# Kernel optimization log

Hardware: AMD Instinct MI355X
Metric: run time of the kernel (lower is better)

## Reference

```python
import jax, jax.numpy as jnp
import numpy as np

N_NODES = 50000


def graph_conv(h, src, dst, W, b, num_nodes):
    """GCN-style conv: transform node features, then sum messages over edges.
    h: [N, Din], W: [Din, Dout] -> out: [N, Dout].
    """
    m = (h @ W)[src]                                   # [E, Dout] per-edge messages
    agg = jax.ops.segment_sum(m, dst, num_segments=num_nodes)  # [N, Dout]
    return agg + b


def setup_inputs() -> dict:
    key = jax.random.key(0)
    ks = jax.random.split(key, 8)
    N, E, D = N_NODES, 800000, 128
    s = 1.0 / np.sqrt(2 * D)
    return {
        "node_feature": jax.random.normal(ks[0], (N, D), jnp.float32),
        "H_prev": jax.random.normal(ks[1], (N, D), jnp.float32),
        "edge_index": jax.random.randint(ks[2], (2, E), 0, N, jnp.int32),
        "W_main": jax.random.normal(ks[3], (D, D), jnp.float32) / np.sqrt(D),
        "b_main": jnp.zeros((D,), jnp.float32),
        "W_z": jax.random.normal(ks[4], (2 * D, D), jnp.float32) * s,
        "b_z": jnp.zeros((D,), jnp.float32),
        "W_r": jax.random.normal(ks[5], (2 * D, D), jnp.float32) * s,
        "b_r": jnp.zeros((D,), jnp.float32),
        "W_h": jax.random.normal(ks[6], (2 * D, D), jnp.float32) * s,
        "b_h": jnp.zeros((D,), jnp.float32),
    }


def reference(node_feature, H_prev, edge_index, W_main, b_main,
              W_z, b_z, W_r, b_r, W_h, b_h):
    N = node_feature.shape[0]
    src, dst = edge_index[0], edge_index[1]
    # main message-passing layer + post-layer activation (ReLU)
    X = jax.nn.relu(graph_conv(node_feature, src, dst, W_main, b_main, N))
    # GRU-gated graph convolutions
    cat_zr = jnp.concatenate([X, H_prev], axis=1)       # [N, 2D]
    Z = jax.nn.sigmoid(graph_conv(cat_zr, src, dst, W_z, b_z, N))
    R = jax.nn.sigmoid(graph_conv(cat_zr, src, dst, W_r, b_r, N))
    cat_h = jnp.concatenate([X, R * H_prev], axis=1)
    H_tilde = jnp.tanh(graph_conv(cat_h, src, dst, W_h, b_h, N))
    H_out = Z * H_prev + (1.0 - Z) * H_tilde
    return H_out
```

## Files before the change

kernel.cpp:

```cpp
#include <hip/hip_runtime.h>
#include <hip/hip_fp16.h>
#include <math.h>

typedef _Float16 f16;
typedef f16 f16x2 __attribute__((ext_vector_type(2)));
typedef f16 f16x4 __attribute__((ext_vector_type(4)));
typedef f16 f16x8 __attribute__((ext_vector_type(8)));
typedef float f32x4_t __attribute__((ext_vector_type(4)));

__device__ __forceinline__ float sigmoidf(float x) {
  return 1.0f / (1.0f + __expf(-x));
}

#define GLDS16(gp, lp)                                                     \
  __builtin_amdgcn_global_load_lds(                                        \
      (const __attribute__((address_space(1))) void*)(gp),                 \
      (__attribute__((address_space(3))) void*)(lp), 16, 0, 0)

__global__ void zero_ints(int* __restrict__ p, int n) {
  int i = blockIdx.x * blockDim.x + threadIdx.x;
  if (i < n) p[i] = 0;
}

__global__ __launch_bounds__(256) void bucket_hist2(const int* __restrict__ dst,
                                                    int* __restrict__ hrows, int E) {
  __shared__ int h[256];
  h[threadIdx.x] = 0;
  __syncthreads();
  int base = blockIdx.x * 4096;
  int lim = min(base + 4096, E);
  for (int e = base + threadIdx.x; e < lim; e += 256)
    atomicAdd(&h[dst[e] >> 8], 1);
  __syncthreads();
  hrows[blockIdx.x * 256 + threadIdx.x] = h[threadIdx.x];
}

__global__ __launch_bounds__(256) void bucket_scan2(const int* __restrict__ hrows,
                                                    int nhb, int* __restrict__ bbases,
                                                    int* __restrict__ gcurP, int NB) {
  __shared__ int wsum[4];
  const int tid = threadIdx.x, lane = tid & 63, wid = tid >> 6;
  int v = 0;
  for (int b = 0; b < nhb; ++b) v += hrows[b * 256 + tid];
  if (tid >= NB) v = 0;
  int x = v;
  #pragma unroll
  for (int d = 1; d < 64; d <<= 1) { int y = __shfl_up(x, d); if (lane >= d) x += y; }
  if (lane == 63) wsum[wid] = x;
  __syncthreads();
  if (wid == 0 && lane < 4) {
    int ws = wsum[lane];
    #pragma unroll
    for (int d = 1; d < 4; d <<= 1) { int y = __shfl_up(ws, d); if (lane >= d) ws += y; }
    wsum[lane] = ws;
  }
  __syncthreads();
  int excl = x - v + (wid ? wsum[wid - 1] : 0);
  if (tid < NB) { bbases[tid] = excl; gcurP[tid * 16] = excl; }
  if (tid == NB - 1) bbases[NB] = excl + v;
}

__global__ __launch_bounds__(256) void partition_v2(const int* __restrict__ src,
                                                    const int* __restrict__ dst,
                                                    int* __restrict__ gcurP,
                                                    unsigned int* __restrict__ bin,
                                                    int E, int NB) {
  __shared__ int bhist[256];
  __shared__ int bofs[257];
  __shared__ int gbase[256];
  __shared__ unsigned int recs[4096];
  const int tid = threadIdx.x;
  const int base = blockIdx.x * 4096;
  bhist[tid] = 0;
  __syncthreads();
  unsigned int rec[16];
  int bk[16];
  #pragma unroll
  for (int k = 0; k < 16; ++k) {
    int e = base + tid + k * 256;
    if (e < E) {
      int d = dst[e];
      rec[k] = (unsigned int)(src[e] & 0xFFFF) | ((unsigned int)(d & 255) << 16);
      bk[k] = d >> 8;
      atomicAdd(&bhist[bk[k]], 1);
    } else {
      bk[k] = -1;
    }
  }
  __syncthreads();
  if (tid < 64) {
    int l = tid;
    int v0 = bhist[4 * l], v1 = bhist[4 * l + 1];
    int v2 = bhist[4 * l + 2], v3 = bhist[4 * l + 3];
    int s1 = v0 + v1, s2 = s1 + v2, t = s2 + v3;
    int x = t;
    #pragma unroll
    for (int d = 1; d < 64; d <<= 1) { int y = __shfl_up(x, d); if (l >= d) x += y; }
    int basex = x - t;
    bofs[4 * l] = basex;
    bofs[4 * l + 1] = basex + v0;
    bofs[4 * l + 2] = basex + s1;
    bofs[4 * l + 3] = basex + s2;
    if (l == 63) bofs[256] = x;
  }
  __syncthreads();
  if (tid < NB && bhist[tid] > 0)
    gbase[tid] = atomicAdd(&gcurP[tid * 16], bhist[tid]);
  bhist[tid] = bofs[tid];
  __syncthreads();
  #pragma unroll
  for (int k = 0; k < 16; ++k) {
    if (bk[k] >= 0) {
      int p = atomicAdd(&bhist[bk[k]], 1);
      recs[p] = rec[k];
    }
  }
  __syncthreads();
  const int total = bofs[256];
  for (int i = tid; i < total; i += 256) {
    int lo = 0, hi = 256;
    #pragma unroll
    for (int s = 0; s < 8; ++s) {
      int mid = (lo + hi) >> 1;
      if (bofs[mid] <= i) lo = mid; else hi = mid;
    }
    bin[gbase[lo] + (i - bofs[lo])] = recs[i];
  }
}

__global__ __launch_bounds__(256) void bucket_sort(const unsigned int* __restrict__ bin,
                                                   const int* __restrict__ bbases,
                                                   unsigned short* __restrict__ eidx,
                                                   int* __restrict__ off,
                                                   int N, int NB) {
  const int b = blockIdx.x;
  const int bb = bbases[b], be = bbases[b + 1];
  const int cntb = be - bb;
  const int d0 = b << 8;
  const int ndst = min(256, N - d0);
  __shared__ int hist[256];
  __shared__ int lofs[256];
  __shared__ int cnt2[256];
  __shared__ unsigned short srt[8192];
  const int tid = threadIdx.x;
  hist[tid] = 0;
  cnt2[tid] = 0;
  __syncthreads();
  for (int i = bb + tid; i < be; i += 256)
    atomicAdd(&hist[(bin[i] >> 16) & 255], 1);
  __syncthreads();
  if (tid < 64) {
    int l = tid;
    int v0 = hist[4 * l], v1 = hist[4 * l + 1], v2 = hist[4 * l + 2], v3 = hist[4 * l + 3];
    int s1 = v0 + v1, s2 = s1 + v2, t = s2 + v3;
    int x = t;
    #pragma unroll
    for (int d = 1; d < 64; d <<= 1) { int y = __shfl_up(x, d); if (l >= d) x += y; }
    int basex = x - t;
    lofs[4 * l] = basex;
    lofs[4 * l + 1] = basex + v0;
    lofs[4 * l + 2] = basex + s1;
    lofs[4 * l + 3] = basex + s2;
  }
  __syncthreads();
  if (tid < ndst) off[d0 + tid] = bb + lofs[tid];
  if (b == NB - 1 && tid == 0) off[N] = be;
  if (cntb <= 8192) {
    for (int i = bb + tid; i < be; i += 256) {
      unsigned int r = bin[i];
      int ld = (r >> 16) & 255;
      int p = lofs[ld] + atomicAdd(&cnt2[ld], 1);
      srt[p] = (unsigned short)(r & 0xFFFF);
    }
    __syncthreads();
    for (int i = tid; i < cntb; i += 256) eidx[bb + i] = srt[i];
  } else {
    for (int i = bb + tid; i < be; i += 256) {
      unsigned int r = bin[i];
      int ld = (r >> 16) & 255;
      int p = bb + lofs[ld] + atomicAdd(&cnt2[ld], 1);
      eidx[p] = (unsigned short)(r & 0xFFFF);
    }
  }
}

__global__ void count_kernel(const int* __restrict__ dst, int* __restrict__ cnt, int E) {
  int base = (blockIdx.x * blockDim.x + threadIdx.x) * 4;
  if (base + 3 < E) {
    int4 d = *(const int4*)&dst[base];
    atomicAdd(&cnt[d.x], 1);
    atomicAdd(&cnt[d.y], 1);
    atomicAdd(&cnt[d.z], 1);
    atomicAdd(&cnt[d.w], 1);
  } else {
    for (int e = base; e < E; ++e) atomicAdd(&cnt[dst[e]], 1);
  }
}

__global__ __launch_bounds__(1024) void scan_local(const int* __restrict__ cnt,
                                                   int* __restrict__ off,
                                                   int* __restrict__ psum, int n) {
  __shared__ int wsum[16];
  const int tid = threadIdx.x, lane = tid & 63, wid = tid >> 6;
  int i = blockIdx.x * 1024 + tid;
  int v = (i < n) ? cnt[i] : 0;
  int x = v;
  #pragma unroll
  for (int d = 1; d < 64; d <<= 1) { int y = __shfl_up(x, d); if (lane >= d) x += y; }
  if (lane == 63) wsum[wid] = x;
  __syncthreads();
  if (wid == 0) {
    int ws = (lane < 16) ? wsum[lane] : 0;
    #pragma unroll
    for (int d = 1; d < 16; d <<= 1) { int y = __shfl_up(ws, d); if (lane >= d) ws += y; }
    if (lane < 16) wsum[lane] = ws;
  }
  __syncthreads();
  int excl = x - v + (wid ? wsum[wid - 1] : 0);
  if (i < n) off[i] = excl;
  if (tid == 1023) psum[blockIdx.x] = wsum[15];
}

__global__ __launch_bounds__(1024) void scan_carry(int* __restrict__ psum,
                                                   int* __restrict__ off,
                                                   int* __restrict__ cur, int nb, int n) {
  __shared__ int wsum[16];
  const int tid = threadIdx.x, lane = tid & 63, wid = tid >> 6;
  int v = (tid < nb) ? psum[tid] : 0;
  int x = v;
  #pragma unroll
  for (int d = 1; d < 64; d <<= 1) { int y = __shfl_up(x, d); if (lane >= d) x += y; }
  if (lane == 63) wsum[wid] = x;
  __syncthreads();
  if (wid == 0) {
    int ws = (lane < 16) ? wsum[lane] : 0;
    #pragma unroll
    for (int d = 1; d < 16; d <<= 1) { int y = __shfl_up(ws, d); if (lane >= d) ws += y; }
    if (lane < 16) wsum[lane] = ws;
  }
  __syncthreads();
  int excl = x - v + (wid ? wsum[wid - 1] : 0);
  if (tid < nb) psum[tid] = excl;
  if (tid == 1023) { off[n] = wsum[15]; cur[n] = wsum[15]; }
}

__global__ __launch_bounds__(1024) void scan_add(int* __restrict__ off, int* __restrict__ cur,
                                                 const int* __restrict__ psum, int n) {
  int i = blockIdx.x * 1024 + threadIdx.x;
  if (i < n) {
    int t = off[i] + psum[blockIdx.x];
    off[i] = t;
    cur[i] = t;
  }
}

__global__ void fill_kernel(const int* __restrict__ src, const int* __restrict__ dst,
                            int* __restrict__ cur, int* __restrict__ eidx, int E) {
  int base = (blockIdx.x * blockDim.x + threadIdx.x) * 4;
  if (base + 3 < E) {
    int4 d = *(const int4*)&dst[base];
    int4 s = *(const int4*)&src[base];
    int p0 = atomicAdd(&cur[d.x], 1);
    int p1 = atomicAdd(&cur[d.y], 1);
    int p2 = atomicAdd(&cur[d.z], 1);
    int p3 = atomicAdd(&cur[d.w], 1);
    eidx[p0] = s.x; eidx[p1] = s.y; eidx[p2] = s.z; eidx[p3] = s.w;
  } else {
    for (int e = base; e < E; ++e) {
      int p = atomicAdd(&cur[dst[e]], 1);
      eidx[p] = src[e];
    }
  }
}

__global__ __launch_bounds__(256) void prep_kernel(
    const float* __restrict__ Wm, const float* __restrict__ Wz,
    const float* __restrict__ Wr, const float* __restrict__ Wh,
    f16* __restrict__ WtM, f16* __restrict__ WtZR, f16* __restrict__ WtH,
    const float* __restrict__ nf, const float* __restrict__ H,
    f16* __restrict__ P0, int N) {
  const int bid = blockIdx.x;
  if (bid < 128) {
    __shared__ float tile[32][33];
    const int t = bid;
    const int x = t & 7, y = (t >> 3) & 3, z = t >> 5;
    const float* W;
    f16* O;
    int K;
    switch (z) {
      case 0: W = Wm; O = WtM; K = 128; break;
      case 1: W = Wz; O = WtZR; K = 256; break;
      case 2: W = Wr; O = WtZR + 128 * 256; K = 256; break;
      default: W = Wh; O = WtH; K = 256; break;
    }
    int bk = x * 32, bn = y * 32;
    if (bk >= K) return;
    int tx = threadIdx.x & 31, ty = threadIdx.x >> 5;
    #pragma unroll
    for (int i = 0; i < 4; ++i)
      tile[ty + 8 * i][tx] = W[(size_t)(bk + ty + 8 * i) * 128 + bn + tx];
    __syncthreads();
    #pragma unroll
    for (int i = 0; i < 4; ++i)
      O[(size_t)(bn + ty + 8 * i) * K + bk + tx] = (f16)tile[tx][ty + 8 * i];
  } else {
    const int w = (bid - 128) * 4 + (threadIdx.x >> 6);
    if (w >= N) return;
    int lane = threadIdx.x & 63;
    const float* S = (lane < 32) ? nf : H;
    int c = (lane & 31) * 4;
    float4 u = *(const float4*)&S[(size_t)w * 128 + c];
    f16x4 o = {(f16)u.x, (f16)u.y, (f16)u.z, (f16)u.w};
    *(f16x4*)&P0[(size_t)w * 256 + (lane < 32 ? 0 : 128) + c] = o;
  }
}

template <int COLS, typename IDX>
__global__ __launch_bounds__(256) void gather(const f16* __restrict__ P,
                                              const int* __restrict__ off,
                                              const IDX* __restrict__ eidx,
                                              f16* __restrict__ O, int N) {
  constexpr int NG = (COLS == 256) ? 2 : 4;
  constexpr int GL = 64 / NG;
  constexpr int SH = (COLS == 256) ? 9 : 8;
  int gid = blockIdx.x * blockDim.x + threadIdx.x;
  int wave = gid >> 6;
  int lane = threadIdx.x & 63;
  int g = lane / GL, lg = lane % GL;
  int node = wave * NG + g;
  if (node >= N) return;
  const int beg = off[node], end = off[node + 1];
  const char* base = (const char*)P + lg * 16;
  float a0 = 0.f, a1 = 0.f, a2 = 0.f, a3 = 0.f;
  float a4 = 0.f, a5 = 0.f, a6 = 0.f, a7 = 0.f;
  int j = beg;
  for (; j + 8 <= end; j += 8) {
    f16x8 v[8];
    #pragma unroll
    for (int u = 0; u < 8; ++u)
      v[u] = *(const f16x8*)(base + (((int)eidx[j + u]) << SH));
    #pragma unroll
    for (int u = 0; u < 8; ++u) {
      a0 += (float)v[u][0]; a1 += (float)v[u][1];
      a2 += (float)v[u][2]; a3 += (float)v[u][3];
      a4 += (float)v[u][4]; a5 += (float)v[u][5];
      a6 += (float)v[u][6]; a7 += (float)v[u][7];
    }
  }
  for (; j < end; ++j) {
    f16x8 v = *(const f16x8*)(base + (((int)eidx[j]) << SH));
    a0 += (float)v[0]; a1 += (float)v[1]; a2 += (float)v[2]; a3 += (float)v[3];
    a4 += (float)v[4]; a5 += (float)v[5]; a6 += (float)v[6]; a7 += (float)v[7];
  }
  f16x8 o = {(f16)a0, (f16)a1, (f16)a2, (f16)a3, (f16)a4, (f16)a5, (f16)a6, (f16)a7};
  *(f16x8*)&O[(size_t)node * COLS + lg * 8] = o;
}

template <int TERMS, int EPI>
__global__ __launch_bounds__(256) void gemm_mfma(
    const f16* __restrict__ A0, int lda0, const f16* __restrict__ A1, int lda1,
    const f16* __restrict__ Wt,
    const float* __restrict__ b0, const float* __restrict__ b1,
    const float* __restrict__ H, const f16* __restrict__ Zh,
    f16* __restrict__ O0, f16* __restrict__ O1, float* __restrict__ Ofp, int N) {
  constexpr int KTOT = TERMS * 128;
  constexpr int T = KTOT / 64;
  __shared__ __align__(16) f16 As[2][64][64];
  __shared__ __align__(16) f16 Bs[2][128][64];
  const int tid = threadIdx.x;
  const int l = tid & 63;
  const int wv = __builtin_amdgcn_readfirstlane(tid >> 6);
  const int fr = l & 15;
  const int q = l >> 4;
  const int brow = blockIdx.x * 64;
  const int coff = blockIdx.y * 128;
  const int rowA = wv * 16 + fr;
  const int sl8 = l >> 3, sg = l & 7;

  f32x4_t acc[8];
  #pragma unroll
  for (int n = 0; n < 8; ++n) acc[n] = (f32x4_t)0.0f;

  auto stage = [&](int t, int buf) {
    const bool sel1 = (TERMS == 2) && (t >= 2);
    const f16* __restrict__ A = sel1 ? A1 : A0;
    const int lda = sel1 ? lda1 : lda0;
    const int klocal = (t & 1) * 64;
    const int kk = t * 64;
    f16* Asf = &As[buf][0][0];
    f16* Bsf = &Bs[buf][0][0];
    #pragma unroll
    for (int c = 0; c < 2; ++c) {
      int chunk = wv + c * 4;
      int row = chunk * 8 + sl8;
      int gs = sg ^ (row & 7);
      int grow = brow + row;
      if (grow > N - 1) grow = N - 1;
      GLDS16(A + (size_t)grow * lda + klocal + gs * 8, Asf + chunk * 512);
    }
    #pragma unroll
    for (int c = 0; c < 4; ++c) {
      int chunk = wv + c * 4;
      int col = chunk * 8 + sl8;
      int gs = sg ^ (col & 7);
      GLDS16(Wt + (size_t)(coff + col) * KTOT + kk + gs * 8, Bsf + chunk * 512);
    }
  };

  stage(0, 0);
  #pragma unroll
  for (int t = 0; t < T; ++t) {
    if (t + 1 < T) {
      stage(t + 1, (t + 1) & 1);
      asm volatile("s_waitcnt vmcnt(6)" ::: "memory");
    } else {
      asm volatile("s_waitcnt vmcnt(0)" ::: "memory");
    }
    __builtin_amdgcn_s_barrier();
    const int buf = t & 1;
    #pragma unroll
    for (int ks = 0; ks < 2; ++ks) {
      f16x8 a = *(const f16x8*)&As[buf][rowA][((ks * 4 + q) ^ (rowA & 7)) * 8];
      f16x8 bfr[8];
      #pragma unroll
      for (int n = 0; n < 8; ++n) {
        int colB = n * 16 + fr;
        bfr[n] = *(const f16x8*)&Bs[buf][colB][((ks * 4 + q) ^ (colB & 7)) * 8];
      }
      #pragma unroll
      for (int n = 0; n < 8; ++n)
        acc[n] = __builtin_amdgcn_mfma_f32_16x16x32_f16(a, bfr[n], acc[n], 0, 0, 0);
    }
    asm volatile("s_waitcnt lgkmcnt(0)" ::: "memory");
    __builtin_amdgcn_s_barrier();
  }

  const int row0 = brow + wv * 16 + q * 4;
  #pragma unroll
  for (int n = 0; n < 8; ++n) {
    int colL = n * 16 + fr;
    if (EPI == 0) {
      float bias = b0[colL];
      #pragma unroll
      for (int r = 0; r < 4; ++r) {
        int row = row0 + r;
        if (row < N)
          O0[(size_t)row * 128 + colL] = (f16)fmaxf(acc[n][r] + bias, 0.f);
      }
    } else if (EPI == 1) {
      if (coff == 0) {
        float bias = b0[colL];
        #pragma unroll
        for (int r = 0; r < 4; ++r) {
          int row = row0 + r;
          if (row < N)
            O0[(size_t)row * 128 + colL] = (f16)sigmoidf(acc[n][r] + bias);
        }
      } else {
        float bias = b1[colL];
        #pragma unroll
        for (int r = 0; r < 4; ++r) {
          int row = row0 + r;
          if (row < N) {
            float g = sigmoidf(acc[n][r] + bias) * H[(size_t)row * 128 + colL];
            O1[(size_t)row * 128 + colL] = (f16)g;
          }
        }
      }
    } else {
      float bias = b0[colL];
      #pragma unroll
      for (int r = 0; r < 4; ++r) {
        int row = row0 + r;
        if (row < N) {
          size_t p = (size_t)row * 128 + colL;
          float ht = tanhf(acc[n][r] + bias);
          float z = (float)Zh[p];
          float h = H[p];
          Ofp[p] = z * h + (1.0f - z) * ht;
        }
      }
    }
  }
}


extern "C" void kernel_launch(void* const* d_in, const int* in_sizes, int n_in,
                              void* d_out, int out_size, void* d_ws, size_t ws_size,
                              hipStream_t stream) {
  const float* nf = (const float*)d_in[0];
  const float* H  = (const float*)d_in[1];
  const int*   ei = (const int*)d_in[2];
  const float* Wm = (const float*)d_in[3];
  const float* bm = (const float*)d_in[4];
  const float* Wz = (const float*)d_in[5];
  const float* bz = (const float*)d_in[6];
  const float* Wr = (const float*)d_in[7];
  const float* br = (const float*)d_in[8];
  const float* Wh = (const float*)d_in[9];
  const float* bh = (const float*)d_in[10];
  float* out = (float*)d_out;

  const int N = in_sizes[0] / 128;
  const int E = in_sizes[2] / 2;
  const int* src = ei;
  const int* dst = ei + E;

  char* ws = (char*)d_ws;
  size_t o = 0;
  auto alloc = [&](size_t bytes) {
    char* p = ws + o;
    o = (o + bytes + 511) & ~(size_t)511;
    return p;
  };
  const int NB = (N + 255) >> 8;
  const int nhb = (E + 4095) / 4096;
  const int nbch = (N + 1023) / 1024;
  int* hrows  = (int*)alloc((size_t)nhb * 256 * 4);
  int* gcurP  = (int*)alloc((size_t)NB * 16 * 4);
  int* bbases = (int*)alloc((size_t)(NB + 1) * 4);
  unsigned int* bin = (unsigned int*)alloc((size_t)E * 4);
  int* off    = (int*)alloc((size_t)(N + 1) * 4);
  int* cur    = (int*)alloc((size_t)(N + 1) * 4);
  int* cnt    = (int*)alloc((size_t)N * 4);
  int* psum   = (int*)alloc((size_t)nbch * 4);
  void* eidx  = (void*)alloc((size_t)E * 4);
  f16* WtM    = (f16*)alloc((size_t)128 * 128 * 2);
  f16* WtZR   = (f16*)alloc((size_t)256 * 256 * 2);
  f16* WtH    = (f16*)alloc((size_t)128 * 256 * 2);
  f16* P0     = (f16*)alloc((size_t)N * 256 * 2);
  f16* X      = (f16*)alloc((size_t)N * 128 * 2);
  f16* AX     = (f16*)alloc((size_t)N * 128 * 2);
  f16* G      = (f16*)alloc((size_t)N * 128 * 2);
  f16* AP0    = (f16*)d_out;
  f16* Zh     = X;
  f16* AG     = P0;

  const bool small = (N <= 65536);

  if (small) {
    bucket_hist2<<<nhb, 256, 0, stream>>>(dst, hrows, E);
    bucket_scan2<<<1, 256, 0, stream>>>(hrows, nhb, bbases, gcurP, NB);
    partition_v2<<<nhb, 256, 0, stream>>>(src, dst, gcurP, bin, E, NB);
    bucket_sort<<<NB, 256, 0, stream>>>(bin, bbases, (unsigned short*)eidx, off, N, NB);
  } else {
    const int qblk = ((E + 3) / 4 + 255) / 256;
    zero_ints<<<(N + 255) / 256, 256, 0, stream>>>(cnt, N);
    count_kernel<<<qblk, 256, 0, stream>>>(dst, cnt, E);
    scan_local<<<nbch, 1024, 0, stream>>>(cnt, off, psum, N);
    scan_carry<<<1, 1024, 0, stream>>>(psum, off, cur, nbch, N);
    scan_add<<<nbch, 1024, 0, stream>>>(off, cur, psum, N);
    fill_kernel<<<qblk, 256, 0, stream>>>(src, dst, cur, (int*)eidx, E);
  }

  prep_kernel<<<128 + (N + 3) / 4, 256, 0, stream>>>(
      Wm, Wz, Wr, Wh, WtM, WtZR, WtH, nf, H, P0, N);

  const int mblk = (N + 63) / 64;
  const int g256 = (N + 7) / 8;
  const int g128 = (N + 15) / 16;

  if (small)
    gather<256, unsigned short><<<g256, 256, 0, stream>>>(P0, off, (const unsigned short*)eidx, AP0, N);
  else
    gather<256, int><<<g256, 256, 0, stream>>>(P0, off, (const int*)eidx, AP0, N);

  gemm_mfma<1, 0><<<dim3(mblk, 1), 256, 0, stream>>>(
      AP0, 256, nullptr, 0, WtM, bm, nullptr, nullptr, nullptr, X, nullptr, nullptr, N);

  if (small)
    gather<128, unsigned short><<<g128, 256, 0, stream>>>(X, off, (const unsigned short*)eidx, AX, N);
  else
    gather<128, int><<<g128, 256, 0, stream>>>(X, off, (const int*)eidx, AX, N);

  gemm_mfma<2, 1><<<dim3(mblk, 2), 256, 0, stream>>>(
      AX, 128, AP0 + 128, 256, WtZR, bz, br, H, nullptr, Zh, G, nullptr, N);

  if (small)
    gather<128, unsigned short><<<g128, 256, 0, stream>>>(G, off, (const unsigned short*)eidx, AG, N);
  else
    gather<128, int><<<g128, 256, 0, stream>>>(G, off, (const int*)eidx, AG, N);

  gemm_mfma<2, 2><<<dim3(mblk, 1), 256, 0, stream>>>(
      AX, 128, AG, 128, WtH, bh, nullptr, H, Zh, nullptr, nullptr, out, N);
}
```

Baseline: 288.9 us.

## Fuse CSR build and weight/feature prep into one cooperative kernel

Result: slower. 367.1 us (+27.1%).

```diff
diff --git a/kernel.cpp b/kernel.cpp
--- a/kernel.cpp
+++ b/kernel.cpp
@@ -1,4 +1,5 @@
 #include <hip/hip_runtime.h>
+#include <hip/hip_cooperative_groups.h>
 #include <hip/hip_fp16.h>
 #include <math.h>
 
@@ -20,6 +21,204 @@
 __global__ void zero_ints(int* __restrict__ p, int n) {
   int i = blockIdx.x * blockDim.x + threadIdx.x;
   if (i < n) p[i] = 0;
+}
+
+__global__ __launch_bounds__(256) void csr_prep_coop(
+    const int* __restrict__ src, const int* __restrict__ dst, int E, int N,
+    int NB, int nhb, int* __restrict__ hrows, int* __restrict__ bbases,
+    int* __restrict__ gcurP, unsigned int* __restrict__ bin,
+    unsigned short* __restrict__ eidx, int* __restrict__ off,
+    const float* __restrict__ Wm, const float* __restrict__ Wz,
+    const float* __restrict__ Wr, const float* __restrict__ Wh,
+    f16* __restrict__ WtM, f16* __restrict__ WtZR, f16* __restrict__ WtH,
+    const float* __restrict__ nf, const float* __restrict__ H,
+    f16* __restrict__ P0) {
+  cooperative_groups::grid_group grid = cooperative_groups::this_grid();
+  const int b = blockIdx.x, tid = threadIdx.x;
+  __shared__ int h[256];
+  __shared__ int bofs[257];
+  __shared__ int gbase[256];
+  __shared__ int wsum4[4];
+  __shared__ unsigned int recs[4096];
+  __shared__ unsigned short srt[8192];
+  __shared__ int lofs[256];
+  __shared__ int cnt2s[256];
+  __shared__ float tile[32][33];
+
+  unsigned int rec[16];
+  int bk[16];
+  h[tid] = 0;
+  __syncthreads();
+  if (b < nhb) {
+    const int base = b * 4096;
+    #pragma unroll
+    for (int k = 0; k < 16; ++k) {
+      int e = base + tid + k * 256;
+      if (e < E) {
+        int d = dst[e];
+        rec[k] = (unsigned int)(src[e] & 0xFFFF) | ((unsigned int)(d & 255) << 16);
+        bk[k] = d >> 8;
+        atomicAdd(&h[bk[k]], 1);
+      } else {
+        bk[k] = -1;
+      }
+    }
+  } else {
+    #pragma unroll
+    for (int k = 0; k < 16; ++k) bk[k] = -1;
+  }
+  __syncthreads();
+  if (b < nhb) hrows[(size_t)b * 256 + tid] = h[tid];
+
+  if (b < 128) {
+    const int x = b & 7, y = (b >> 3) & 3, z = b >> 5;
+    const float* W;
+    f16* O;
+    int K;
+    switch (z) {
+      case 0: W = Wm; O = WtM; K = 128; break;
+      case 1: W = Wz; O = WtZR; K = 256; break;
+      case 2: W = Wr; O = WtZR + 128 * 256; K = 256; break;
+      default: W = Wh; O = WtH; K = 256; break;
+    }
+    int bkk = x * 32, bn = y * 32;
+    if (bkk < K) {
+      int tx = tid & 31, ty = tid >> 5;
+      #pragma unroll
+      for (int i = 0; i < 4; ++i)
+        tile[ty + 8 * i][tx] = W[(size_t)(bkk + ty + 8 * i) * 128 + bn + tx];
+      __syncthreads();
+      #pragma unroll
+      for (int i = 0; i < 4; ++i)
+        O[(size_t)(bn + ty + 8 * i) * K + bkk + tx] = (f16)tile[tx][ty + 8 * i];
+    }
+  }
+  {
+    const int wv = tid >> 6, lane = tid & 63;
+    const float* S = (lane < 32) ? nf : H;
+    const int c = (lane & 31) * 4;
+    const int coloff = (lane < 32) ? 0 : 128;
+    for (int w = b * 4 + wv; w < N; w += gridDim.x * 4) {
+      float4 u = *(const float4*)&S[(size_t)w * 128 + c];
+      f16x4 o = {(f16)u.x, (f16)u.y, (f16)u.z, (f16)u.w};
+      *(f16x4*)&P0[(size_t)w * 256 + coloff + c] = o;
+    }
+  }
+
+  grid.sync();
+
+  if (b == 0) {
+    int v = 0;
+    for (int b2 = 0; b2 < nhb; ++b2) v += hrows[(size_t)b2 * 256 + tid];
+    if (tid >= NB) v = 0;
+    const int lane = tid & 63, wid = tid >> 6;
+    int x = v;
+    #pragma unroll
+    for (int d = 1; d < 64; d <<= 1) { int y = __shfl_up(x, d); if (lane >= d) x += y; }
+    if (lane == 63) wsum4[wid] = x;
+    __syncthreads();
+    if (wid == 0 && lane < 4) {
+      int wsv = wsum4[lane];
+      #pragma unroll
+      for (int d = 1; d < 4; d <<= 1) { int y = __shfl_up(wsv, d); if (lane >= d) wsv += y; }
+      wsum4[lane] = wsv;
+    }
+    __syncthreads();
+    int excl = x - v + (wid ? wsum4[wid - 1] : 0);
+    if (tid < NB) { bbases[tid] = excl; gcurP[tid * 16] = excl; }
+    if (tid == NB - 1) bbases[NB] = excl + v;
+  }
+
+  grid.sync();
+
+  if (b < nhb) {
+    if (tid < 64) {
+      int l = tid;
+      int v0 = h[4 * l], v1 = h[4 * l + 1], v2 = h[4 * l + 2], v3 = h[4 * l + 3];
+      int s1 = v0 + v1, s2 = s1 + v2, t = s2 + v3;
+      int x = t;
+      #pragma unroll
+      for (int d = 1; d < 64; d <<= 1) { int y = __shfl_up(x, d); if (l >= d) x += y; }
+      int basex = x - t;
+      bofs[4 * l] = basex;
+      bofs[4 * l + 1] = basex + v0;
+      bofs[4 * l + 2] = basex + s1;
+      bofs[4 * l + 3] = basex + s2;
+      if (l == 63) bofs[256] = x;
+    }
+    __syncthreads();
+    if (tid < NB && h[tid] > 0)
+      gbase[tid] = atomicAdd(&gcurP[tid * 16], h[tid]);
+    __syncthreads();
+    h[tid] = bofs[tid];
+    __syncthreads();
+    #pragma unroll
+    for (int k = 0; k < 16; ++k) {
+      if (bk[k] >= 0) {
+        int p = atomicAdd(&h[bk[k]], 1);
+        recs[p] = rec[k];
+      }
+    }
+    __syncthreads();
+    const int total = bofs[256];
+    for (int i = tid; i < total; i += 256) {
+      int lo = 0, hi = 256;
+      #pragma unroll
+      for (int s = 0; s < 8; ++s) {
+        int mid = (lo + hi) >> 1;
+        if (bofs[mid] <= i) lo = mid; else hi = mid;
+      }
+      bin[gbase[lo] + (i - bofs[lo])] = recs[i];
+    }
+  }
+
+  grid.sync();
+
+  if (b < NB) {
+    const int bb = bbases[b], be = bbases[b + 1];
+    const int cntb = be - bb;
+    const int d0 = b << 8;
+    const int ndst = min(256, N - d0);
+    h[tid] = 0;
+    cnt2s[tid] = 0;
+    __syncthreads();
+    for (int i = bb + tid; i < be; i += 256)
+      atomicAdd(&h[(bin[i] >> 16) & 255], 1);
+    __syncthreads();
+    if (tid < 64) {
+      int l = tid;
+      int v0 = h[4 * l], v1 = h[4 * l + 1], v2 = h[4 * l + 2], v3 = h[4 * l + 3];
+      int s1 = v0 + v1, s2 = s1 + v2, t = s2 + v3;
+      int x = t;
+      #pragma unroll
+      for (int d = 1; d < 64; d <<= 1) { int y = __shfl_up(x, d); if (l >= d) x += y; }
+      int basex = x - t;
+      lofs[4 * l] = basex;
+      lofs[4 * l + 1] = basex + v0;
+      lofs[4 * l + 2] = basex + s1;
+      lofs[4 * l + 3] = basex + s2;
+    }
+    __syncthreads();
+    if (tid < ndst) off[d0 + tid] = bb + lofs[tid];
+    if (b == NB - 1 && tid == 0) off[N] = be;
+    if (cntb <= 8192) {
+      for (int i = bb + tid; i < be; i += 256) {
+        unsigned int r = bin[i];
+        int ld = (r >> 16) & 255;
+        int p = lofs[ld] + atomicAdd(&cnt2s[ld], 1);
+        srt[p] = (unsigned short)(r & 0xFFFF);
+      }
+      __syncthreads();
+      for (int i = tid; i < cntb; i += 256) eidx[bb + i] = srt[i];
+    } else {
+      for (int i = bb + tid; i < be; i += 256) {
+        unsigned int r = bin[i];
+        int ld = (r >> 16) & 255;
+        int p = bb + lofs[ld] + atomicAdd(&cnt2s[ld], 1);
+        eidx[p] = (unsigned short)(r & 0xFFFF);
+      }
+    }
+  }
 }
 
 __global__ __launch_bounds__(256) void bucket_hist2(const int* __restrict__ dst,
@@ -106,6 +305,7 @@
   __syncthreads();
   if (tid < NB && bhist[tid] > 0)
     gbase[tid] = atomicAdd(&gcurP[tid * 16], bhist[tid]);
+  __syncthreads();
   bhist[tid] = bofs[tid];
   __syncthreads();
   #pragma unroll
@@ -361,7 +561,7 @@
     const f16* __restrict__ A0, int lda0, const f16* __restrict__ A1, int lda1,
     const f16* __restrict__ Wt,
     const float* __restrict__ b0, const float* __restrict__ b1,
-    const float* __restrict__ H, const f16* __restrict__ Zh,
+    const f16* __restrict__ Hh, const f16* __restrict__ Zh,
     f16* __restrict__ O0, f16* __restrict__ O1, float* __restrict__ Ofp, int N) {
   constexpr int KTOT = TERMS * 128;
   constexpr int T = KTOT / 64;
@@ -462,7 +662,8 @@
         for (int r = 0; r < 4; ++r) {
           int row = row0 + r;
           if (row < N) {
-            float g = sigmoidf(acc[n][r] + bias) * H[(size_t)row * 128 + colL];
+            float hv = (float)Hh[(size_t)row * 256 + colL];
+            float g = sigmoidf(acc[n][r] + bias) * hv;
             O1[(size_t)row * 128 + colL] = (f16)g;
           }
         }
@@ -473,11 +674,10 @@
       for (int r = 0; r < 4; ++r) {
         int row = row0 + r;
         if (row < N) {
-          size_t p = (size_t)row * 128 + colL;
           float ht = tanhf(acc[n][r] + bias);
-          float z = (float)Zh[p];
-          float h = H[p];
-          Ofp[p] = z * h + (1.0f - z) * ht;
+          float z = (float)Zh[(size_t)row * 128 + colL];
+          float hv = (float)Hh[(size_t)row * 256 + colL];
+          Ofp[(size_t)row * 128 + colL] = z * hv + (1.0f - z) * ht;
         }
       }
     }
@@ -532,29 +732,59 @@
   f16* X      = (f16*)alloc((size_t)N * 128 * 2);
   f16* AX     = (f16*)alloc((size_t)N * 128 * 2);
   f16* G      = (f16*)alloc((size_t)N * 128 * 2);
+  f16* AG     = (f16*)alloc((size_t)N * 128 * 2);
   f16* AP0    = (f16*)d_out;
   f16* Zh     = X;
-  f16* AG     = P0;
+  const f16* Hh = P0 + 128;
 
   const bool small = (N <= 65536);
 
+  bool coop_done = false;
   if (small) {
-    bucket_hist2<<<nhb, 256, 0, stream>>>(dst, hrows, E);
-    bucket_scan2<<<1, 256, 0, stream>>>(hrows, nhb, bbases, gcurP, NB);
-    partition_v2<<<nhb, 256, 0, stream>>>(src, dst, gcurP, bin, E, NB);
-    bucket_sort<<<NB, 256, 0, stream>>>(bin, bbases, (unsigned short*)eidx, off, N, NB);
-  } else {
-    const int qblk = ((E + 3) / 4 + 255) / 256;
-    zero_ints<<<(N + 255) / 256, 256, 0, stream>>>(cnt, N);
-    count_kernel<<<qblk, 256, 0, stream>>>(dst, cnt, E);
-    scan_local<<<nbch, 1024, 0, stream>>>(cnt, off, psum, N);
-    scan_carry<<<1, 1024, 0, stream>>>(psum, off, cur, nbch, N);
-    scan_add<<<nbch, 1024, 0, stream>>>(off, cur, psum, N);
-    fill_kernel<<<qblk, 256, 0, stream>>>(src, dst, cur, (int*)eidx, E);
-  }
-
-  prep_kernel<<<128 + (N + 3) / 4, 256, 0, stream>>>(
-      Wm, Wz, Wr, Wh, WtM, WtZR, WtH, nf, H, P0, N);
+    const int NBLK = (nhb > NB) ? nhb : NB;
+    const int* src_a = src; const int* dst_a = dst;
+    int E_a = E, N_a = N, NB_a = NB, nhb_a = nhb;
+    unsigned short* eidx_a = (unsigned short*)eidx;
+    const float* Wm_a = Wm; const float* Wz_a = Wz;
+    const float* Wr_a = Wr; const float* Wh_a = Wh;
+    const float* nf_a = nf; const float* H_a = H;
+    f16* WtM_a = WtM; f16* WtZR_a = WtZR; f16* WtH_a = WtH; f16* P0_a = P0;
+    int* hrows_a = hrows; int* bbases_a = bbases; int* gcurP_a = gcurP;
+    unsigned int* bin_a = bin; int* off_a = off;
+    void* kargs[] = {
+      (void*)&src_a, (void*)&dst_a, (void*)&E_a, (void*)&N_a,
+      (void*)&NB_a, (void*)&nhb_a, (void*)&hrows_a, (void*)&bbases_a,
+      (void*)&gcurP_a, (void*)&bin_a, (void*)&eidx_a, (void*)&off_a,
+      (void*)&Wm_a, (void*)&Wz_a, (void*)&Wr_a, (void*)&Wh_a,
+      (void*)&WtM_a, (void*)&WtZR_a, (void*)&WtH_a,
+      (void*)&nf_a, (void*)&H_a, (void*)&P0_a
+    };
+    hipError_t ce = hipLaunchCooperativeKernel((const void*)csr_prep_coop,
+                                               dim3(NBLK), dim3(256), kargs, 0, stream);
+    if (ce == hipSuccess) {
+      coop_done = true;
+    } else {
+      (void)hipGetLastError();
+    }
+  }
+  if (!coop_done) {
+    if (small) {
+      bucket_hist2<<<nhb, 256, 0, stream>>>(dst, hrows, E);
+      bucket_scan2<<<1, 256, 0, stream>>>(hrows, nhb, bbases, gcurP, NB);
+      partition_v2<<<nhb, 256, 0, stream>>>(src, dst, gcurP, bin, E, NB);
+      bucket_sort<<<NB, 256, 0, stream>>>(bin, bbases, (unsigned short*)eidx, off, N, NB);
+    } else {
+      const int qblk = ((E + 3) / 4 + 255) / 256;
+      zero_ints<<<(N + 255) / 256, 256, 0, stream>>>(cnt, N);
+      count_kernel<<<qblk, 256, 0, stream>>>(dst, cnt, E);
+      scan_local<<<nbch, 1024, 0, stream>>>(cnt, off, psum, N);
+      scan_carry<<<1, 1024, 0, stream>>>(psum, off, cur, nbch, N);
+      scan_add<<<nbch, 1024, 0, stream>>>(off, cur, psum, N);
+      fill_kernel<<<qblk, 256, 0, stream>>>(src, dst, cur, (int*)eidx, E);
+    }
+    prep_kernel<<<128 + (N + 3) / 4, 256, 0, stream>>>(
+        Wm, Wz, Wr, Wh, WtM, WtZR, WtH, nf, H, P0, N);
+  }
 
   const int mblk = (N + 63) / 64;
   const int g256 = (N + 7) / 8;
@@ -574,7 +804,7 @@
     gather<128, int><<<g128, 256, 0, stream>>>(X, off, (const int*)eidx, AX, N);
 
   gemm_mfma<2, 1><<<dim3(mblk, 2), 256, 0, stream>>>(
-      AX, 128, AP0 + 128, 256, WtZR, bz, br, H, nullptr, Zh, G, nullptr, N);
+      AX, 128, AP0 + 128, 256, WtZR, bz, br, Hh, nullptr, Zh, G, nullptr, N);
 
   if (small)
     gather<128, unsigned short><<<g128, 256, 0, stream>>>(G, off, (const unsigned short*)eidx, AG, N);
@@ -582,5 +812,5 @@
     gather<128, int><<<g128, 256, 0, stream>>>(G, off, (const int*)eidx, AG, N);
 
   gemm_mfma<2, 2><<<dim3(mblk, 1), 256, 0, stream>>>(
-      AX, 128, AG, 128, WtH, bh, nullptr, H, Zh, nullptr, nullptr, out, N);
-}
+      AX, 128, AG, 128, WtH, bh, nullptr, Hh, Zh, nullptr, nullptr, out, N);
+}
```
